# Kernel optimization log

Hardware: AMD Instinct MI355X
Metric: run time of the kernel (lower is better)

The kernel has to match this reference:

```python
import jax, jax.numpy as jnp
import numpy as np

N_GRAPHS = 50
EPS = 1e-5
N_NODES, N_EDGES, F, L, N_HEADS = 50000, 800000, 64, 3, 3


def _bn(x, gamma, beta):
    # BatchNorm1d over nodes, training-mode (biased batch statistics)
    m = x.mean(axis=0)
    v = jnp.mean((x - m) ** 2, axis=0)
    return gamma * (x - m) * jax.lax.rsqrt(v + EPS) + beta


def _pna_layer(x, src, dst, preW, preb, postW, postb, linW, linb, avg_log, avg_lin):
    N = x.shape[0]
    # pre-MLP on concatenated (target x_i, source x_j): [E, 2F] -> [E, F]
    h = jnp.concatenate([x[dst], x[src]], axis=-1) @ preW + preb
    ones = jnp.ones((h.shape[0],), h.dtype)
    cnt = jax.ops.segment_sum(ones, dst, num_segments=N)[:, None]
    has = cnt > 0
    deg = jnp.maximum(cnt, 1.0)  # PNAConv clamps degree to >= 1
    mean = jax.ops.segment_sum(h, dst, num_segments=N) / deg
    mean2 = jax.ops.segment_sum(h * h, dst, num_segments=N) / deg
    std = jnp.sqrt(jax.nn.relu(mean2 - mean * mean) + EPS)
    mn = jnp.where(has, jax.ops.segment_min(h, dst, num_segments=N), 0.0)
    mx = jnp.where(has, jax.ops.segment_max(h, dst, num_segments=N), 0.0)
    aggr = jnp.concatenate([mean, mn, mx, std], axis=-1)  # [N, 4F]
    log_deg = jnp.log(deg + 1.0)
    out = jnp.concatenate([aggr,
                           aggr * (log_deg / avg_log),   # amplification
                           aggr * (avg_log / log_deg),   # attenuation
                           aggr * (deg / avg_lin)],      # linear
                          axis=-1)                       # [N, 16F]
    out = jnp.concatenate([x, out], axis=-1) @ postW + postb  # post-MLP [N, F]
    return out @ linW + linb


def _forward(x, deg_hist, preW, preb, postW, postb, linW, linb, bn_g, bn_b,
             sharedW, sharedb, hW1, hb1, hW2, hb2, hW3, hb3, src, dst, batch):
    bins = jnp.arange(deg_hist.shape[0], dtype=deg_hist.dtype)
    tot = deg_hist.sum()
    avg_lin = (bins * deg_hist).sum() / tot
    avg_log = (jnp.log(bins + 1.0) * deg_hist).sum() / tot
    for l in range(preW.shape[0]):  # only num_conv_layers convs run (zip truncation)
        x = _pna_layer(x, src, dst, preW[l], preb[l], postW[l], postb[l],
                       linW[l], linb[l], avg_log, avg_lin)
        x = jax.nn.relu(_bn(x, bn_g[l], bn_b[l]))
    gcnt = jax.ops.segment_sum(jnp.ones((x.shape[0],), x.dtype), batch,
                               num_segments=N_GRAPHS)[:, None]
    g = jax.ops.segment_sum(x, batch, num_segments=N_GRAPHS) / jnp.maximum(gcnt, 1.0)
    g = jax.nn.relu(g @ sharedW + sharedb)  # shared MLP (num_shared=1)
    h1 = jax.nn.relu(jnp.einsum('gd,hdk->hgk', g, hW1) + hb1[:, None, :])
    h2 = jax.nn.relu(jnp.einsum('hgk,hkm->hgm', h1, hW2) + hb2[:, None, :])
    o = jnp.einsum('hgm,hmo->hgo', h2, hW3) + hb3[:, None, :]  # [H, G, 1]
    return jnp.transpose(o[..., 0])  # [G, H] == torch.cat(head outputs, dim=1)


def setup_inputs():
    key = jax.random.key(0)
    ks = jax.random.split(key, 12)

    def w(k, shape, fan_in):
        return jax.random.normal(k, shape, jnp.float32) / np.sqrt(fan_in)

    return {
        "x": jax.random.normal(ks[0], (N_NODES, F), jnp.float32),
        "edge_index": jax.random.randint(ks[1], (2, N_EDGES), 0, N_NODES),
        "batch": jnp.sort(jax.random.randint(ks[2], (N_NODES,), 0, N_GRAPHS)),
        "deg_hist": jax.random.uniform(ks[3], (33,), jnp.float32) + 0.01,
        "preW": w(ks[4], (L, 2 * F, F), 2 * F),
        "preb": jnp.zeros((L, F), jnp.float32),
        "postW": w(ks[5], (L, 17 * F, F), 17 * F),
        "postb": jnp.zeros((L, F), jnp.float32),
        "linW": w(ks[6], (L, F, F), F),
        "linb": jnp.zeros((L, F), jnp.float32),
        "bn_g": jnp.ones((L, F), jnp.float32),
        "bn_b": jnp.zeros((L, F), jnp.float32),
        "sharedW": w(ks[7], (F, F), F),
        "sharedb": jnp.zeros((F,), jnp.float32),
        "hW1": w(ks[8], (N_HEADS, F, 50), F),
        "hb1": jnp.zeros((N_HEADS, 50), jnp.float32),
        "hW2": w(ks[9], (N_HEADS, 50, 25), 50),
        "hb2": jnp.zeros((N_HEADS, 25), jnp.float32),
        "hW3": w(ks[10], (N_HEADS, 25, 1), 25),
        "hb3": jnp.zeros((N_HEADS, 1), jnp.float32),
    }


def reference(x, edge_index, batch, deg_hist, preW, preb, postW, postb,
              linW, linb, bn_g, bn_b, sharedW, sharedb,
              hW1, hb1, hW2, hb2, hW3, hb3):
    return _forward(x, deg_hist, preW, preb, postW, postb, linW, linb,
                    bn_g, bn_b, sharedW, sharedb, hW1, hb1, hW2, hb2,
                    hW3, hb3, edge_index[0], edge_index[1], batch)
```

## Files before the change

kernel.cpp:

```cpp
#include <hip/hip_runtime.h>
#include <math.h>

#define N_NODES 50000
#define N_EDGES 800000
#define NGRAPHS 50
#define NHEADS 3
#define EPS 1e-5f
#define NWIN 196
#define WSH 8

typedef _Float16 half8 __attribute__((ext_vector_type(8)));
typedef _Float16 half2v __attribute__((ext_vector_type(2)));
typedef float f32x4 __attribute__((ext_vector_type(4)));

__device__ inline half2v h2_shfl_xor(half2v v, int m) {
  int xi = __shfl_xor(*(int*)&v, m, 64);
  return *(half2v*)&xi;
}

__global__ void __launch_bounds__(256) k_zero_setup(int* cnt, float* gsum, float* gcnt,
                                                    float* part, float* partq,
                                                    const float* dh, int nbins, float* scal) {
  int gid = blockIdx.x * 256 + threadIdx.x;
  int gs = gridDim.x * 256;
  for (int i = gid; i < N_NODES; i += gs) cnt[i] = 0;
  for (int i = gid; i < NGRAPHS * 64; i += gs) gsum[i] = 0.f;
  for (int i = gid; i < NGRAPHS; i += gs) gcnt[i] = 0.f;
  for (int i = gid; i < 3 * 128 * 64; i += gs) { part[i] = 0.f; partq[i] = 0.f; }
  if (blockIdx.x == 0 && threadIdx.x < 64) {
    int t = threadIdx.x;
    float v = (t < nbins) ? dh[t] : 0.f;
    float lv = logf((float)t + 1.f) * v;
    float bv = (float)t * v;
    for (int d = 32; d > 0; d >>= 1) {
      v  += __shfl_down(v,  d, 64);
      lv += __shfl_down(lv, d, 64);
      bv += __shfl_down(bv, d, 64);
    }
    if (t == 0) { scal[0] = lv / v; scal[1] = bv / v; }
  }
}

__global__ void __launch_bounds__(256) k_hist(const int* __restrict__ dst, int* __restrict__ cnt) {
  int e = blockIdx.x * 256 + threadIdx.x;
  if (e < N_EDGES) atomicAdd(&cnt[dst[e]], 1);
}

__global__ void __launch_bounds__(256) k_scan_a(const int* __restrict__ cnt, int* __restrict__ off,
                                                int* __restrict__ blksum) {
  __shared__ int lds[256];
  int t = threadIdx.x;
  int base = blockIdx.x * 1024 + t * 4;
  int v0 = (base + 0 < N_NODES) ? cnt[base + 0] : 0;
  int v1 = (base + 1 < N_NODES) ? cnt[base + 1] : 0;
  int v2 = (base + 2 < N_NODES) ? cnt[base + 2] : 0;
  int v3 = (base + 3 < N_NODES) ? cnt[base + 3] : 0;
  int tsum = v0 + v1 + v2 + v3;
  lds[t] = tsum; __syncthreads();
  for (int d = 1; d < 256; d <<= 1) {
    int x = (t >= d) ? lds[t - d] : 0;
    __syncthreads();
    lds[t] += x;
    __syncthreads();
  }
  int run = lds[t] - tsum;
  if (base + 0 < N_NODES) off[base + 0] = run; run += v0;
  if (base + 1 < N_NODES) off[base + 1] = run; run += v1;
  if (base + 2 < N_NODES) off[base + 2] = run; run += v2;
  if (base + 3 < N_NODES) off[base + 3] = run;
  if (t == 255) blksum[blockIdx.x] = lds[255];
}

__global__ void __launch_bounds__(64) k_scan_b(const int* __restrict__ blksum, int* __restrict__ blkoff) {
  int t = threadIdx.x;
  int own = (t < 49) ? blksum[t] : 0;
  int v = own;
  for (int d = 1; d < 64; d <<= 1) {
    int u = __shfl_up(v, d, 64);
    if (t >= d) v += u;
  }
  if (t < 49) blkoff[t] = v - own;
}

__global__ void __launch_bounds__(256) k_scan_c(int* __restrict__ off, const int* __restrict__ blkoff,
                                                int* __restrict__ wincur) {
  int i = blockIdx.x * 256 + threadIdx.x;
  if (i < N_NODES) {
    int fo = off[i] + blkoff[i >> 10];
    off[i] = fo;
    if ((i & 255) == 0) wincur[i >> WSH] = fo;
  }
  if (i == 0) off[N_NODES] = N_EDGES;
}

__global__ void __launch_bounds__(256) k_part1(const int* __restrict__ src, const int* __restrict__ dst,
                                               int* __restrict__ wincur, int* __restrict__ pairS,
                                               unsigned char* __restrict__ pairDL) {
  __shared__ int hist[256];
  __shared__ int scan[256];
  __shared__ int baseg[256];
  __shared__ int place[256];
  __shared__ int sS[2048];
  __shared__ unsigned char sDL[2048];
  __shared__ unsigned char sW[2048];
  int t = threadIdx.x;
  int base = blockIdx.x * 2048;
  hist[t] = 0;
  __syncthreads();
  int d[8], s[8];
  #pragma unroll
  for (int i = 0; i < 8; ++i) {
    int e = base + t + 256 * i;
    bool val = e < N_EDGES;
    d[i] = val ? dst[e] : -1;
    s[i] = val ? src[e] : 0;
    if (val) atomicAdd(&hist[d[i] >> WSH], 1);
  }
  __syncthreads();
  int v = hist[t];
  scan[t] = v; __syncthreads();
  for (int dd = 1; dd < 256; dd <<= 1) {
    int x = (t >= dd) ? scan[t - dd] : 0;
    __syncthreads();
    scan[t] += x;
    __syncthreads();
  }
  place[t] = scan[t] - v;
  if (v > 0) baseg[t] = atomicAdd(&wincur[t], v);
  __syncthreads();
  #pragma unroll
  for (int i = 0; i < 8; ++i) {
    if (d[i] >= 0) {
      int w = d[i] >> WSH;
      int p = atomicAdd(&place[w], 1);
      sS[p] = s[i] << 7;
      sDL[p] = (unsigned char)(d[i] & 255);
      sW[p] = (unsigned char)w;
    }
  }
  __syncthreads();
  int tot = min(N_EDGES - base, 2048);
  for (int i = t; i < tot; i += 256) {
    int w = sW[i];
    int gidx = baseg[w] + (i - (scan[w] - hist[w]));
    pairS[gidx] = sS[i];
    pairDL[gidx] = sDL[i];
  }
}

__global__ void __launch_bounds__(256) k_part2(const int* __restrict__ off, const int* __restrict__ pairS,
                                               const unsigned char* __restrict__ pairDL,
                                               int* __restrict__ esrc) {
  __shared__ int curW[256];
  __shared__ int offW[257];
  __shared__ int esrcW[6144];
  int w = blockIdx.x, t = threadIdx.x;
  int n0 = w << WSH;
  offW[t] = off[min(n0 + t, N_NODES)];
  if (t == 0) offW[256] = off[min(n0 + 256, N_NODES)];
  curW[t] = 0;
  __syncthreads();
  int start = offW[0];
  int end = offW[256];
  int cnt = end - start;
  if (cnt <= 6144) {
    for (int i = t; i < cnt; i += 256) {
      int s = pairS[start + i];
      int dl = pairDL[start + i];
      int pos = offW[dl] - start + atomicAdd(&curW[dl], 1);
      esrcW[pos] = s;
    }
    __syncthreads();
    for (int i = t; i < cnt; i += 256) esrc[start + i] = esrcW[i];
  } else {
    for (int i = t; i < cnt; i += 256) {
      int s = pairS[start + i];
      int dl = pairDL[start + i];
      int pos = offW[dl] + atomicAdd(&curW[dl], 1);
      esrc[pos] = s;
    }
  }
}

__global__ void __launch_bounds__(256) k_prep(const float* __restrict__ xin, _Float16* __restrict__ xout,
                                              const float* __restrict__ preW, const float* __restrict__ postW,
                                              const float* __restrict__ linW, _Float16* __restrict__ preP,
                                              _Float16* __restrict__ postAP, _Float16* __restrict__ postBP,
                                              _Float16* __restrict__ linP) {
  int t0 = blockIdx.x * 256 + threadIdx.x;
  if (t0 < 400000) {
    const float* s = xin + (size_t)t0 * 8;
    float4 v0 = *(const float4*)s;
    float4 v1 = *(const float4*)(s + 4);
    half8 h = {(_Float16)v0.x, (_Float16)v0.y, (_Float16)v0.z, (_Float16)v0.w,
               (_Float16)v1.x, (_Float16)v1.y, (_Float16)v1.z, (_Float16)v1.w};
    *(half8*)(xout + (size_t)t0 * 8) = h;
    return;
  }
  int t = t0 - 400000;
  if (t < 24576) {
    int l = t >> 13, r = t & 8191;
    int j = r & 7, lane = (r >> 3) & 63, ctg = (r >> 9) & 7, kc = r >> 12;
    int k = kc * 32 + ((lane >> 4) << 3) + j;
    int col = ctg * 16 + (lane & 15);
    const float* W = preW + (size_t)l * 8192;
    float v = (col < 64) ? W[k * 64 + col] : W[(64 + k) * 64 + (col - 64)];
    preP[(size_t)l * 8192 + r] = (_Float16)v;
  } else if (t < 221184) {
    int q = t - 24576;
    int l = q >> 16, r = q & 65535;
    int j = r & 7, lane = (r >> 3) & 63, ct = (r >> 9) & 3, s = (r >> 11) & 3, kc = r >> 13;
    int k = kc * 32 + ((lane >> 4) << 3) + j;
    int col = ct * 16 + (lane & 15);
    postAP[(size_t)l * 65536 + r] = (_Float16)postW[(size_t)l * 69632 + (size_t)(64 + s * 256 + k) * 64 + col];
  } else if (t < 233472) {
    int q = t - 221184;
    int l = q >> 12, r = q & 4095;
    int j = r & 7, lane = (r >> 3) & 63, ct = (r >> 9) & 3, kc = r >> 11;
    int k = kc * 32 + ((lane >> 4) << 3) + j;
    int col = ct * 16 + (lane & 15);
    postBP[(size_t)l * 4096 + r] = (_Float16)postW[(size_t)l * 69632 + (size_t)k * 64 + col];
  } else if (t < 245760) {
    int q = t - 233472;
    int l = q >> 12, r = q & 4095;
    int j = r & 7, lane = (r >> 3) & 63, ct = (r >> 9) & 3, kc = r >> 11;
    int k = kc * 32 + ((lane >> 4) << 3) + j;
    int col = ct * 16 + (lane & 15);
    linP[(size_t)l * 4096 + r] = (_Float16)linW[(size_t)l * 4096 + (size_t)k * 64 + col];
  }
}

__global__ void __launch_bounds__(256) k_mfma_g1(const _Float16* __restrict__ yin,
                                                 const float* __restrict__ part, const float* __restrict__ partq,
                                                 const float* __restrict__ bng, const float* __restrict__ bnb,
                                                 int applyBN,
                                                 const _Float16* __restrict__ wp, const float* __restrict__ bias,
                                                 _Float16* __restrict__ Aout, _Float16* __restrict__ Bout,
                                                 _Float16* __restrict__ xout) {
  __shared__ float ls[256], lq[256];
  __shared__ __align__(16) float scS[64], shS[64];
  int t = threadIdx.x, lane = t & 63, wave = t >> 6;
  int r0 = blockIdx.x * 64;
  int mrow = lane & 15, q8 = ((lane >> 4) << 3);
  if (applyBN) {
    int col = t & 63, qtr = t >> 6;
    float s = 0.f, q = 0.f;
    for (int i = 0; i < 32; ++i) {
      int slot = qtr * 32 + i;
      s += part[slot * 64 + col];
      q += partq[slot * 64 + col];
    }
    ls[t] = s; lq[t] = q; __syncthreads();
    if (t < 64) {
      s = ls[t] + ls[64 + t] + ls[128 + t] + ls[192 + t];
      q = lq[t] + lq[64 + t] + lq[128 + t] + lq[192 + t];
      float m = s / (float)N_NODES;
      float v = fmaxf(q / (float)N_NODES - m * m, 0.f);
      float sc = bng[t] * rsqrtf(v + EPS);
      scS[t] = sc;
      shS[t] = bnb[t] - m * sc;
    }
    __syncthreads();
  }
  f32x4 acc[4][2];
  #pragma unroll
  for (int rt = 0; rt < 4; ++rt) { acc[rt][0] = (f32x4)0.f; acc[rt][1] = (f32x4)0.f; }
  #pragma unroll
  for (int kc = 0; kc < 2; ++kc) {
    int k0 = kc * 32 + q8;
    half8 a[4];
    #pragma unroll
    for (int rt = 0; rt < 4; ++rt) {
      int r = min(r0 + rt * 16 + mrow, N_NODES - 1);
      a[rt] = *(const half8*)(yin + (size_t)r * 64 + k0);
    }
    if (applyBN) {
      float4 sc0 = *(const float4*)(scS + k0);
      float4 sc1 = *(const float4*)(scS + k0 + 4);
      float4 sh0 = *(const float4*)(shS + k0);
      float4 sh1 = *(const float4*)(shS + k0 + 4);
      #pragma unroll
      for (int rt = 0; rt < 4; ++rt) {
        half8 v = a[rt];
        v[0] = (_Float16)fmaxf((float)v[0] * sc0.x + sh0.x, 0.f);
        v[1] = (_Float16)fmaxf((float)v[1] * sc0.y + sh0.y, 0.f);
        v[2] = (_Float16)fmaxf((float)v[2] * sc0.z + sh0.z, 0.f);
        v[3] = (_Float16)fmaxf((float)v[3] * sc0.w + sh0.w, 0.f);
        v[4] = (_Float16)fmaxf((float)v[4] * sc1.x + sh1.x, 0.f);
        v[5] = (_Float16)fmaxf((float)v[5] * sc1.y + sh1.y, 0.f);
        v[6] = (_Float16)fmaxf((float)v[6] * sc1.z + sh1.z, 0.f);
        v[7] = (_Float16)fmaxf((float)v[7] * sc1.w + sh1.w, 0.f);
        a[rt] = v;
      }
      if (wave == 0) {
        #pragma unroll
        for (int rt = 0; rt < 4; ++rt) {
          int r = min(r0 + rt * 16 + mrow, N_NODES - 1);
          *(half8*)(xout + (size_t)r * 64 + k0) = a[rt];
        }
      }
    }
    #pragma unroll
    for (int ci = 0; ci < 2; ++ci) {
      int ctg = wave * 2 + ci;
      half8 b = *(const half8*)(wp + (size_t)((kc * 8 + ctg) * 64 + lane) * 8);
      #pragma unroll
      for (int rt = 0; rt < 4; ++rt)
        acc[rt][ci] = __builtin_amdgcn_mfma_f32_16x16x32_f16(a[rt], b, acc[rt][ci], 0, 0, 0);
    }
  }
  #pragma unroll
  for (int ci = 0; ci < 2; ++ci) {
    int col = (wave * 2 + ci) * 16 + mrow;
    bool isA = col < 64;
    float bv = isA ? bias[col] : 0.f;
    _Float16* outp = isA ? (Aout + col) : (Bout + (col - 64));
    #pragma unroll
    for (int rt = 0; rt < 4; ++rt)
      #pragma unroll
      for (int reg = 0; reg < 4; ++reg) {
        int row = r0 + rt * 16 + ((lane >> 4) << 2) + reg;
        if (row < N_NODES) outp[(size_t)row * 64] = (_Float16)(acc[rt][ci][reg] + bv);
      }
  }
}

__global__ void __launch_bounds__(256) k_aggr(const _Float16* __restrict__ A, const _Float16* __restrict__ B,
                                              const int* __restrict__ off, const int* __restrict__ esrc,
                                              const float* __restrict__ scal, _Float16* __restrict__ aggr,
                                              float4* __restrict__ scales) {
  int wave = threadIdx.x >> 6, lane = threadIdx.x & 63;
  int n = blockIdx.x * 4 + wave;
  int lh = lane & 31, eg = lane >> 5;
  half2v c2 = *(const half2v*)(A + (size_t)n * 64 + lh * 2);
  int e0 = __builtin_amdgcn_readfirstlane(off[n]);
  int e1 = __builtin_amdgcn_readfirstlane(off[n + 1]);
  int deg = e1 - e0;
  const char* Bb = (const char*)B;
  int lo4 = lh * 4;
  const _Float16 HMAX = (_Float16)65504.f;
  half2v z2 = {(_Float16)0.f, (_Float16)0.f};
  half2v p2 = {HMAX, HMAX};
  half2v m2v = {-HMAX, -HMAX};
  half2v s2 = z2, q2 = z2, mn2 = p2, mx2 = m2v;
  if (deg > 0) {
    int e1m1 = e1 - 1;
    for (int e = e0; e < e1; e += 16) {
      int ro[8];
      #pragma unroll
      for (int g = 0; g < 8; ++g)
        ro[g] = esrc[min(e + g * 2 + eg, e1m1)];
      half2v v[8];
      #pragma unroll
      for (int g = 0; g < 8; ++g)
        v[g] = *(const half2v*)(Bb + ro[g] + lo4);
      #pragma unroll
      for (int g = 0; g < 8; ++g) {
        bool valid = (e + g * 2 + eg) < e1;
        half2v vm = valid ? v[g] : z2;
        s2 += vm;
        q2 += vm * vm;
        mn2 = __builtin_elementwise_min(mn2, valid ? v[g] : p2);
        mx2 = __builtin_elementwise_max(mx2, valid ? v[g] : m2v);
      }
    }
  }
  s2 += h2_shfl_xor(s2, 32);
  q2 += h2_shfl_xor(q2, 32);
  mn2 = __builtin_elementwise_min(mn2, h2_shfl_xor(mn2, 32));
  mx2 = __builtin_elementwise_max(mx2, h2_shfl_xor(mx2, 32));
  if (eg == 0) {
    _Float16* arow = aggr + (size_t)n * 256;
    half2v w;
    if (deg == 0) {
      w = z2;
      *(half2v*)(arow + lh * 2) = w;
      *(half2v*)(arow + 64 + lh * 2) = w;
      *(half2v*)(arow + 128 + lh * 2) = w;
      w[0] = (_Float16)sqrtf(EPS); w[1] = w[0];
      *(half2v*)(arow + 192 + lh * 2) = w;
    } else {
      float c0 = (float)c2[0], c1 = (float)c2[1];
      float inv = 1.f / (float)deg;
      float mb0 = (float)s2[0] * inv, mb1 = (float)s2[1] * inv;
      float v0 = fmaxf((float)q2[0] * inv - mb0 * mb0, 0.f);
      float v1 = fmaxf((float)q2[1] * inv - mb1 * mb1, 0.f);
      w[0] = (_Float16)(c0 + mb0); w[1] = (_Float16)(c1 + mb1);
      *(half2v*)(arow + lh * 2) = w;
      w[0] = (_Float16)(c0 + (float)mn2[0]); w[1] = (_Float16)(c1 + (float)mn2[1]);
      *(half2v*)(arow + 64 + lh * 2) = w;
      w[0] = (_Float16)(c0 + (float)mx2[0]); w[1] = (_Float16)(c1 + (float)mx2[1]);
      *(half2v*)(arow + 128 + lh * 2) = w;
      w[0] = (_Float16)sqrtf(v0 + EPS); w[1] = (_Float16)sqrtf(v1 + EPS);
      *(half2v*)(arow + 192 + lh * 2) = w;
    }
    if (lane == 0) {
      float degf = fmaxf((float)deg, 1.f);
      float ld = logf(degf + 1.f);
      float al = scal[0], av = scal[1];
      scales[n] = make_float4(ld / al, al / ld, degf / av, 0.f);
    }
  }
}

__global__ void __launch_bounds__(256) k_mfma_g23(const _Float16* __restrict__ aggr,
                                                  const _Float16* __restrict__ x16,
                                                  const _Float16* __restrict__ wpA, const _Float16* __restrict__ wpB,
                                                  const float* __restrict__ postb, const float4* __restrict__ scales,
                                                  const _Float16* __restrict__ linP, const float* __restrict__ linb,
                                                  _Float16* __restrict__ y16,
                                                  float* __restrict__ part, float* __restrict__ partq) {
  __shared__ _Float16 yS[64][72];
  int t = threadIdx.x, lane = t & 63, ct = t >> 6;
  int r0 = blockIdx.x * 64;
  int mrow = lane & 15, q8 = ((lane >> 4) << 3);
  f32x4 acc[4][4];
  #pragma unroll
  for (int rt = 0; rt < 4; ++rt)
    #pragma unroll
    for (int s = 0; s < 4; ++s) acc[rt][s] = (f32x4)0.f;
  #pragma unroll 2
  for (int kc = 0; kc < 8; ++kc) {
    half8 a[4];
    #pragma unroll
    for (int rt = 0; rt < 4; ++rt) {
      int r = min(r0 + rt * 16 + mrow, N_NODES - 1);
      a[rt] = *(const half8*)(aggr + (size_t)r * 256 + kc * 32 + q8);
    }
    #pragma unroll
    for (int s = 0; s < 4; ++s) {
      half8 b = *(const half8*)(wpA + (size_t)((((kc * 4 + s) * 4 + ct) * 64) + lane) * 8);
      #pragma unroll
      for (int rt = 0; rt < 4; ++rt)
        acc[rt][s] = __builtin_amdgcn_mfma_f32_16x16x32_f16(a[rt], b, acc[rt][s], 0, 0, 0);
    }
  }
  #pragma unroll
  for (int kc = 0; kc < 2; ++kc) {
    half8 a[4];
    #pragma unroll
    for (int rt = 0; rt < 4; ++rt) {
      int r = min(r0 + rt * 16 + mrow, N_NODES - 1);
      a[rt] = *(const half8*)(x16 + (size_t)r * 64 + kc * 32 + q8);
    }
    half8 b = *(const half8*)(wpB + (size_t)(((kc * 4 + ct) * 64) + lane) * 8);
    #pragma unroll
    for (int rt = 0; rt < 4; ++rt)
      acc[rt][0] = __builtin_amdgcn_mfma_f32_16x16x32_f16(a[rt], b, acc[rt][0], 0, 0, 0);
  }
  int col = ct * 16 + mrow;
  float pb = postb[col];
  #pragma unroll
  for (int rt = 0; rt < 4; ++rt)
    #pragma unroll
    for (int reg = 0; reg < 4; ++reg) {
      int rr = rt * 16 + ((lane >> 4) << 2) + reg;
      int row = min(r0 + rr, N_NODES - 1);
      float4 sc = scales[row];
      float v = acc[rt][0][reg] + sc.x * acc[rt][1][reg] + sc.y * acc[rt][2][reg] + sc.z * acc[rt][3][reg] + pb;
      yS[rr][col] = (_Float16)v;
    }
  __syncthreads();
  f32x4 acc2[4];
  #pragma unroll
  for (int rt = 0; rt < 4; ++rt) acc2[rt] = (f32x4)0.f;
  #pragma unroll
  for (int kc = 0; kc < 2; ++kc) {
    half8 a[4];
    #pragma unroll
    for (int rt = 0; rt < 4; ++rt)
      a[rt] = *(const half8*)(&yS[rt * 16 + mrow][kc * 32 + q8]);
    half8 b = *(const half8*)(linP + (size_t)(((kc * 4 + ct) * 64) + lane) * 8);
    #pragma unroll
    for (int rt = 0; rt < 4; ++rt)
      acc2[rt] = __builtin_amdgcn_mfma_f32_16x16x32_f16(a[rt], b, acc2[rt], 0, 0, 0);
  }
  float bv = linb[col];
  float s = 0.f, q = 0.f;
  #pragma unroll
  for (int rt = 0; rt < 4; ++rt)
    #pragma unroll
    for (int reg = 0; reg < 4; ++reg) {
      int row = r0 + rt * 16 + ((lane >> 4) << 2) + reg;
      if (row < N_NODES) {
        float v = acc2[rt][reg] + bv;
        y16[(size_t)row * 64 + col] = (_Float16)v;
        s += v; q += v * v;
      }
    }
  int slot = (blockIdx.x & 127) * 64 + col;
  atomicAdd(&part[slot], s);
  atomicAdd(&partq[slot], q);
}

__global__ void __launch_bounds__(256) k_pool(const _Float16* __restrict__ y16,
                                              const float* __restrict__ part, const float* __restrict__ partq,
                                              const float* __restrict__ bng, const float* __restrict__ bnb,
                                              const int* __restrict__ batch,
                                              float* __restrict__ gsum, float* __restrict__ gcnt) {
  __shared__ float ls[256], lq[256];
  __shared__ float scS[64], shS[64];
  int t = threadIdx.x, col = t & 63, rl = t >> 6;
  {
    float s = 0.f, q = 0.f;
    for (int i = 0; i < 32; ++i) {
      int slot = rl * 32 + i;
      s += part[slot * 64 + col];
      q += partq[slot * 64 + col];
    }
    ls[t] = s; lq[t] = q; __syncthreads();
    if (t < 64) {
      s = ls[t] + ls[64 + t] + ls[128 + t] + ls[192 + t];
      q = lq[t] + lq[64 + t] + lq[128 + t] + lq[192 + t];
      float m = s / (float)N_NODES;
      float v = fmaxf(q / (float)N_NODES - m * m, 0.f);
      float sc = bng[t] * rsqrtf(v + EPS);
      scS[t] = sc;
      shS[t] = bnb[t] - m * sc;
    }
    __syncthreads();
  }
  float sc = scS[col], sh = shS[col];
  int rbeg = blockIdx.x * 64 + rl * 16;
  int rend = min(rbeg + 16, N_NODES);
  int curg = -1, cr = 0;
  float acc = 0.f;
  for (int r = rbeg; r < rend; ++r) {
    int g = batch[r];
    if (g != curg) {
      if (curg >= 0) {
        atomicAdd(&gsum[curg * 64 + col], acc);
        if (col == 0) atomicAdd(&gcnt[curg], (float)cr);
      }
      curg = g; acc = 0.f; cr = 0;
    }
    acc += fmaxf((float)y16[(size_t)r * 64 + col] * sc + sh, 0.f); cr++;
  }
  if (curg >= 0) {
    atomicAdd(&gsum[curg * 64 + col], acc);
    if (col == 0) atomicAdd(&gcnt[curg], (float)cr);
  }
}

__global__ void __launch_bounds__(64) k_sharedheads(const float* __restrict__ gsum, const float* __restrict__ gcnt,
                                                    const float* __restrict__ W, const float* __restrict__ b,
                                                    const float* __restrict__ hW1, const float* __restrict__ hb1,
                                                    const float* __restrict__ hW2, const float* __restrict__ hb2,
                                                    const float* __restrict__ hW3, const float* __restrict__ hb3,
                                                    float* __restrict__ out) {
  __shared__ float gm[64], gv[64], h1[50], h2[25];
  int bid = blockIdx.x;
  int g = bid / NHEADS, h = bid % NHEADS;
  int t = threadIdx.x;
  float cv = fmaxf(gcnt[g], 1.f);
  gm[t] = gsum[g * 64 + t] / cv;
  __syncthreads();
  float s0 = b[t];
  for (int k = 0; k < 64; ++k) s0 += gm[k] * W[k * 64 + t];
  gv[t] = fmaxf(s0, 0.f);
  __syncthreads();
  if (t < 50) {
    float s = hb1[h * 50 + t];
    for (int k = 0; k < 64; ++k) s += gv[k] * hW1[h * 3200 + k * 50 + t];
    h1[t] = fmaxf(s, 0.f);
  }
  __syncthreads();
  if (t < 25) {
    float s = hb2[h * 25 + t];
    for (int k = 0; k < 50; ++k) s += h1[k] * hW2[h * 1250 + k * 25 + t];
    h2[t] = fmaxf(s, 0.f);
  }
  __syncthreads();
  if (t == 0) {
    float s = hb3[h];
    for (int k = 0; k < 25; ++k) s += h2[k] * hW3[h * 25 + k];
    out[g * NHEADS + h] = s;
  }
}

extern "C" void kernel_launch(void* const* d_in, const int* in_sizes, int n_in,
                              void* d_out, int out_size, void* d_ws, size_t ws_size,
                              hipStream_t stream) {
  const float* x0    = (const float*)d_in[0];
  const int*   eidx  = (const int*)d_in[1];
  const int*   batch = (const int*)d_in[2];
  const float* dh    = (const float*)d_in[3];
  const float* preW  = (const float*)d_in[4];
  const float* preb  = (const float*)d_in[5];
  const float* postW = (const float*)d_in[6];
  const float* postb = (const float*)d_in[7];
  const float* linW  = (const float*)d_in[8];
  const float* linb  = (const float*)d_in[9];
  const float* bng   = (const float*)d_in[10];
  const float* bnb   = (const float*)d_in[11];
  const float* shW   = (const float*)d_in[12];
  const float* shb   = (const float*)d_in[13];
  const float* hW1   = (const float*)d_in[14];
  const float* hb1   = (const float*)d_in[15];
  const float* hW2   = (const float*)d_in[16];
  const float* hb2   = (const float*)d_in[17];
  const float* hW3   = (const float*)d_in[18];
  const float* hb3   = (const float*)d_in[19];
  float* out = (float*)d_out;

  char* ws = (char*)d_ws;
  size_t o = 0;
  auto alloc = [&](size_t bytes) {
    char* p = ws + o;
    o = (o + bytes + 255) & ~(size_t)255;
    return p;
  };
  float* scal   = (float*)alloc(8 * 4);
  int* off      = (int*)alloc((N_NODES + 1) * 4);
  int* cnt      = (int*)alloc(N_NODES * 4);
  int* esrc     = (int*)alloc(N_EDGES * 4);
  int* pairS    = (int*)alloc(N_EDGES * 4);
  unsigned char* pairDL = (unsigned char*)alloc(N_EDGES);
  int* wincur   = (int*)alloc(NWIN * 4);
  int* blks     = (int*)alloc(64 * 4);
  int* blko     = (int*)alloc(64 * 4);
  _Float16* A16    = (_Float16*)alloc((size_t)N_NODES * 64 * 2 + 256 * 16);
  _Float16* B16    = (_Float16*)alloc((size_t)N_NODES * 64 * 2 + 256 * 16);
  _Float16* aggr16 = (_Float16*)alloc((size_t)N_NODES * 256 * 2 + 256 * 16);
  _Float16* x16a   = (_Float16*)alloc((size_t)N_NODES * 64 * 2 + 256 * 16);
  _Float16* xbuf   = (_Float16*)alloc((size_t)N_NODES * 64 * 2 + 256 * 16);
  _Float16* y16    = (_Float16*)alloc((size_t)N_NODES * 64 * 2 + 256 * 16);
  float4* scales = (float4*)alloc((size_t)N_NODES * 16);
  _Float16* preP   = (_Float16*)alloc(3 * 8192 * 2);
  _Float16* postAP = (_Float16*)alloc((size_t)3 * 65536 * 2);
  _Float16* postBP = (_Float16*)alloc(3 * 4096 * 2);
  _Float16* linP   = (_Float16*)alloc(3 * 4096 * 2);
  float* part   = (float*)alloc(3 * 128 * 64 * 4);
  float* partq  = (float*)alloc(3 * 128 * 64 * 4);
  float* gsum   = (float*)alloc(NGRAPHS * 64 * 4);
  float* gcnt   = (float*)alloc(NGRAPHS * 4);

  const int* srcv = eidx;
  const int* dstv = eidx + N_EDGES;

  k_zero_setup<<<256, 256, 0, stream>>>(cnt, gsum, gcnt, part, partq, dh, in_sizes[3], scal);
  k_hist<<<(N_EDGES + 255) / 256, 256, 0, stream>>>(dstv, cnt);
  k_scan_a<<<49, 256, 0, stream>>>(cnt, off, blks);
  k_scan_b<<<1, 64, 0, stream>>>(blks, blko);
  k_scan_c<<<196, 256, 0, stream>>>(off, blko, wincur);
  k_part1<<<(N_EDGES + 2047) / 2048, 256, 0, stream>>>(srcv, dstv, wincur, pairS, pairDL);
  k_part2<<<NWIN, 256, 0, stream>>>(off, pairS, pairDL, esrc);
  k_prep<<<(400000 + 245760 + 255) / 256, 256, 0, stream>>>(x0, x16a, preW, postW, linW,
                                                            preP, postAP, postBP, linP);

  for (int l = 0; l < 3; ++l) {
    const _Float16* g1in = (l == 0) ? x16a : y16;
    const _Float16* xc   = (l == 0) ? x16a : xbuf;
    const float* partP  = part + (size_t)(l == 0 ? 0 : l - 1) * 8192;
    const float* partqP = partq + (size_t)(l == 0 ? 0 : l - 1) * 8192;
    k_mfma_g1<<<782, 256, 0, stream>>>(g1in, partP, partqP,
                                       bng + (l == 0 ? 0 : (l - 1) * 64), bnb + (l == 0 ? 0 : (l - 1) * 64),
                                       (l > 0) ? 1 : 0,
                                       preP + (size_t)l * 8192, preb + l * 64, A16, B16, xbuf);
    k_aggr<<<12500, 256, 0, stream>>>(A16, B16, off, esrc, scal, aggr16, scales);
    k_mfma_g23<<<782, 256, 0, stream>>>(aggr16, xc, postAP + (size_t)l * 65536,
                                        postBP + (size_t)l * 4096, postb + l * 64, scales,
                                        linP + (size_t)l * 4096, linb + l * 64, y16,
                                        part + (size_t)l * 8192, partq + (size_t)l * 8192);
  }
  k_pool<<<782, 256, 0, stream>>>(y16, part + 2 * 8192, partq + 2 * 8192,
                                  bng + 2 * 64, bnb + 2 * 64, batch, gsum, gcnt);
  k_sharedheads<<<NGRAPHS * NHEADS, 64, 0, stream>>>(gsum, gcnt, shW, shb,
                                                     hW1, hb1, hW2, hb2, hW3, hb3, out);
}
```

Before: 450.7 us.

## Halve g23 row tile, preload all A fragments, and reduce BN-stat atomics per wave

The post/lin MFMA kernel now processes 32 rows per block instead of 64, doubling the grid to 1563 blocks so more waves are resident across CUs. All aggr and x A-fragments are loaded up front into registers, so the loads are issued early and can overlap. Before the atomics, the per-column BN partial sums are reduced across the four row groups of a wave with shuffles, which cuts global atomic traffic by a factor of four. The trade-offs are that each wave reuses the weight B-fragments across fewer rows, and the large preloaded register set may raise VGPR pressure.

```diff
diff --git a/kernel.cpp b/kernel.cpp
--- a/kernel.cpp
+++ b/kernel.cpp
@@ -410,48 +410,51 @@
                                                   const _Float16* __restrict__ linP, const float* __restrict__ linb,
                                                   _Float16* __restrict__ y16,
                                                   float* __restrict__ part, float* __restrict__ partq) {
-  __shared__ _Float16 yS[64][72];
+  __shared__ _Float16 yS[32][72];
   int t = threadIdx.x, lane = t & 63, ct = t >> 6;
-  int r0 = blockIdx.x * 64;
+  int r0 = blockIdx.x * 32;
   int mrow = lane & 15, q8 = ((lane >> 4) << 3);
-  f32x4 acc[4][4];
-  #pragma unroll
-  for (int rt = 0; rt < 4; ++rt)
+  int r[2];
+  #pragma unroll
+  for (int rt = 0; rt < 2; ++rt) r[rt] = min(r0 + rt * 16 + mrow, N_NODES - 1);
+  half8 a[8][2];
+  #pragma unroll
+  for (int kc = 0; kc < 8; ++kc)
+    #pragma unroll
+    for (int rt = 0; rt < 2; ++rt)
+      a[kc][rt] = *(const half8*)(aggr + (size_t)r[rt] * 256 + kc * 32 + q8);
+  half8 ax[2][2];
+  #pragma unroll
+  for (int kc = 0; kc < 2; ++kc)
+    #pragma unroll
+    for (int rt = 0; rt < 2; ++rt)
+      ax[kc][rt] = *(const half8*)(x16 + (size_t)r[rt] * 64 + kc * 32 + q8);
+  f32x4 acc[2][4];
+  #pragma unroll
+  for (int rt = 0; rt < 2; ++rt)
     #pragma unroll
     for (int s = 0; s < 4; ++s) acc[rt][s] = (f32x4)0.f;
-  #pragma unroll 2
+  #pragma unroll
   for (int kc = 0; kc < 8; ++kc) {
-    half8 a[4];
-    #pragma unroll
-    for (int rt = 0; rt < 4; ++rt) {
-      int r = min(r0 + rt * 16 + mrow, N_NODES - 1);
-      a[rt] = *(const half8*)(aggr + (size_t)r * 256 + kc * 32 + q8);
-    }
     #pragma unroll
     for (int s = 0; s < 4; ++s) {
       half8 b = *(const half8*)(wpA + (size_t)((((kc * 4 + s) * 4 + ct) * 64) + lane) * 8);
       #pragma unroll
-      for (int rt = 0; rt < 4; ++rt)
-        acc[rt][s] = __builtin_amdgcn_mfma_f32_16x16x32_f16(a[rt], b, acc[rt][s], 0, 0, 0);
+      for (int rt = 0; rt < 2; ++rt)
+        acc[rt][s] = __builtin_amdgcn_mfma_f32_16x16x32_f16(a[kc][rt], b, acc[rt][s], 0, 0, 0);
     }
   }
   #pragma unroll
   for (int kc = 0; kc < 2; ++kc) {
-    half8 a[4];
-    #pragma unroll
-    for (int rt = 0; rt < 4; ++rt) {
-      int r = min(r0 + rt * 16 + mrow, N_NODES - 1);
-      a[rt] = *(const half8*)(x16 + (size_t)r * 64 + kc * 32 + q8);
-    }
     half8 b = *(const half8*)(wpB + (size_t)(((kc * 4 + ct) * 64) + lane) * 8);
     #pragma unroll
-    for (int rt = 0; rt < 4; ++rt)
-      acc[rt][0] = __builtin_amdgcn_mfma_f32_16x16x32_f16(a[rt], b, acc[rt][0], 0, 0, 0);
+    for (int rt = 0; rt < 2; ++rt)
+      acc[rt][0] = __builtin_amdgcn_mfma_f32_16x16x32_f16(ax[kc][rt], b, acc[rt][0], 0, 0, 0);
   }
   int col = ct * 16 + mrow;
   float pb = postb[col];
   #pragma unroll
-  for (int rt = 0; rt < 4; ++rt)
+  for (int rt = 0; rt < 2; ++rt)
     #pragma unroll
     for (int reg = 0; reg < 4; ++reg) {
       int rr = rt * 16 + ((lane >> 4) << 2) + reg;
@@ -461,24 +464,24 @@
       yS[rr][col] = (_Float16)v;
     }
   __syncthreads();
-  f32x4 acc2[4];
-  #pragma unroll
-  for (int rt = 0; rt < 4; ++rt) acc2[rt] = (f32x4)0.f;
+  f32x4 acc2[2];
+  #pragma unroll
+  for (int rt = 0; rt < 2; ++rt) acc2[rt] = (f32x4)0.f;
   #pragma unroll
   for (int kc = 0; kc < 2; ++kc) {
-    half8 a[4];
-    #pragma unroll
-    for (int rt = 0; rt < 4; ++rt)
-      a[rt] = *(const half8*)(&yS[rt * 16 + mrow][kc * 32 + q8]);
+    half8 av[2];
+    #pragma unroll
+    for (int rt = 0; rt < 2; ++rt)
+      av[rt] = *(const half8*)(&yS[rt * 16 + mrow][kc * 32 + q8]);
     half8 b = *(const half8*)(linP + (size_t)(((kc * 4 + ct) * 64) + lane) * 8);
     #pragma unroll
-    for (int rt = 0; rt < 4; ++rt)
-      acc2[rt] = __builtin_amdgcn_mfma_f32_16x16x32_f16(a[rt], b, acc2[rt], 0, 0, 0);
+    for (int rt = 0; rt < 2; ++rt)
+      acc2[rt] = __builtin_amdgcn_mfma_f32_16x16x32_f16(av[rt], b, acc2[rt], 0, 0, 0);
   }
   float bv = linb[col];
   float s = 0.f, q = 0.f;
   #pragma unroll
-  for (int rt = 0; rt < 4; ++rt)
+  for (int rt = 0; rt < 2; ++rt)
     #pragma unroll
     for (int reg = 0; reg < 4; ++reg) {
       int row = r0 + rt * 16 + ((lane >> 4) << 2) + reg;
@@ -488,9 +491,13 @@
         s += v; q += v * v;
       }
     }
-  int slot = (blockIdx.x & 127) * 64 + col;
-  atomicAdd(&part[slot], s);
-  atomicAdd(&partq[slot], q);
+  s += __shfl_xor(s, 16, 64); s += __shfl_xor(s, 32, 64);
+  q += __shfl_xor(q, 16, 64); q += __shfl_xor(q, 32, 64);
+  if ((lane >> 4) == 0) {
+    int slot = (blockIdx.x & 127) * 64 + col;
+    atomicAdd(&part[slot], s);
+    atomicAdd(&partq[slot], q);
+  }
 }
 
 __global__ void __launch_bounds__(256) k_pool(const _Float16* __restrict__ y16,
@@ -658,10 +665,10 @@
                                        (l > 0) ? 1 : 0,
                                        preP + (size_t)l * 8192, preb + l * 64, A16, B16, xbuf);
     k_aggr<<<12500, 256, 0, stream>>>(A16, B16, off, esrc, scal, aggr16, scales);
-    k_mfma_g23<<<782, 256, 0, stream>>>(aggr16, xc, postAP + (size_t)l * 65536,
-                                        postBP + (size_t)l * 4096, postb + l * 64, scales,
-                                        linP + (size_t)l * 4096, linb + l * 64, y16,
-                                        part + (size_t)l * 8192, partq + (size_t)l * 8192);
+    k_mfma_g23<<<1563, 256, 0, stream>>>(aggr16, xc, postAP + (size_t)l * 65536,
+                                         postBP + (size_t)l * 4096, postb + l * 64, scales,
+                                         linP + (size_t)l * 4096, linb + l * 64, y16,
+                                         part + (size_t)l * 8192, partq + (size_t)l * 8192);
   }
   k_pool<<<782, 256, 0, stream>>>(y16, part + 2 * 8192, partq + 2 * 8192,
                                   bng + 2 * 64, bnb + 2 * 64, batch, gsum, gcnt);
```

Result: faster. 431.5 us, median of 2 (-4.3%).
